# Optimization experiments

Measured on AMD Instinct MI355X. Metric: run time of the kernel, lower is better.

The kernel has to match this reference:

```python
import jax, jax.numpy as jnp
import numpy as np

CH = 256  # channels

def setup_inputs() -> dict:
    key = jax.random.key(0)
    ks = jax.random.split(key, 9)
    B, H, W = 8, 64, 64
    c8, c2 = CH // 8, CH // 2
    s = lambda fan_in: 1.0 / np.sqrt(fan_in)
    return {
        "x": jax.random.normal(ks[0], (B, H, W, CH), dtype=jnp.float32),
        "Wq": jax.random.normal(ks[1], (CH, c8), dtype=jnp.float32) * s(CH),
        "bq": jnp.zeros((c8,), dtype=jnp.float32),
        "Wk": jax.random.normal(ks[2], (CH, c8), dtype=jnp.float32) * s(CH),
        "bk": jnp.zeros((c8,), dtype=jnp.float32),
        "Wv": jax.random.normal(ks[3], (CH, c2), dtype=jnp.float32) * s(CH),
        "bv": jnp.zeros((c2,), dtype=jnp.float32),
        "Wo": jax.random.normal(ks[4], (c2, CH), dtype=jnp.float32) * s(c2),
        "bo": jnp.zeros((CH,), dtype=jnp.float32),
    }

def reference(x, Wq, bq, Wk, bk, Wv, bv, Wo, bo):
    B, H, W, C = x.shape
    # 1x1 convs are per-pixel matmuls over the channel dim
    q = x @ Wq + bq                      # [B,H,W,C/8]
    k = x @ Wk + bk                      # [B,H,W,C/8]
    v = x @ Wv + bv                      # [B,H,W,C/2]
    N = H * W
    qf = q.reshape(B, N, -1)
    kf = k.reshape(B, N, -1)
    vf = v.reshape(B, N, -1)
    # full self-attention over flattened spatial positions (no scaling, per source)
    scores = jnp.einsum('bnd,bmd->bnm', qf, kf)   # [B,N,N]
    attn = jax.nn.softmax(scores, axis=-1)
    out = jnp.einsum('bnm,bmd->bnd', attn, vf)    # [B,N,C/2]
    out = out.reshape(B, H, W, -1)
    return out @ Wo + bo + x
```

## Files before the change

### kernel.cpp

```cpp
#include <hip/hip_runtime.h>

typedef __attribute__((ext_vector_type(8))) short short8;
typedef __attribute__((ext_vector_type(4))) float f32x4;
typedef __attribute__((ext_vector_type(16))) float f32x16;

__device__ __forceinline__ unsigned short f2bf(float f) {
  unsigned int u = __float_as_uint(f);
  u += 0x7fffu + ((u >> 16) & 1u);
  return (unsigned short)(u >> 16);
}
__device__ __forceinline__ float bf2f(unsigned short h) {
  return __uint_as_float(((unsigned int)h) << 16);
}
__device__ __forceinline__ unsigned int cvtpk(float a, float b) {
  unsigned int r;
  asm("v_cvt_pk_bf16_f32 %0, %1, %2" : "=v"(r) : "v"(a), "v"(b));
  return r;
}
__device__ __forceinline__ float lo16f(unsigned int u) { return __uint_as_float(u << 16); }
__device__ __forceinline__ float hi16f(unsigned int u) { return __uint_as_float(u & 0xffff0000u); }
__device__ __forceinline__ short8 ld8(const unsigned short* p) {
  return *(const short8*)p;
}
__device__ __forceinline__ int swap23(int x) {
  return (x & 0x13) | ((x & 4) << 1) | ((x & 8) >> 1);
}
#define MFMA(a, b, c) __builtin_amdgcn_mfma_f32_16x16x32_bf16((a), (b), (c), 0, 0, 0)
#define MFMA32(a, b, c) __builtin_amdgcn_mfma_f32_32x32x16_bf16((a), (b), (c), 0, 0, 0)
#define LOG2E 1.4426950408889634f

typedef const __attribute__((address_space(1))) unsigned int* gas_u32p;
typedef __attribute__((address_space(3))) unsigned int* las_u32p;

__global__ void prep_weights(const float* __restrict__ Wq, const float* __restrict__ Wk,
                             const float* __restrict__ Wv, const float* __restrict__ Wo,
                             unsigned short* __restrict__ Wth, unsigned short* __restrict__ Wtl,
                             unsigned short* __restrict__ WoT) {
  int idx = blockIdx.x * 256 + threadIdx.x;
  if (idx < 192 * 256) {
    int o = idx >> 8, c = idx & 255;
    float w = (o < 32) ? Wq[c * 32 + o] : (o < 64) ? Wk[c * 32 + (o - 32)] : Wv[c * 128 + (o - 64)];
    unsigned short h = f2bf(w);
    Wth[idx] = h;
    Wtl[idx] = f2bf(w - bf2f(h));
  } else if (idx < 192 * 256 + 256 * 128) {
    int j = idx - 192 * 256;
    int c = j >> 7, d = j & 127;
    WoT[j] = f2bf(Wo[d * 256 + c]);
  }
}

__global__ __launch_bounds__(256) void proj_qkv(
    const float* __restrict__ x,
    const unsigned short* __restrict__ Wth, const unsigned short* __restrict__ Wtl,
    const float* __restrict__ bq, const float* __restrict__ bk, const float* __restrict__ bv,
    unsigned short* __restrict__ qh, unsigned short* __restrict__ qlo,
    unsigned short* __restrict__ KVF) {
  __shared__ unsigned short xsh[32][264];
  __shared__ unsigned short xsl[32][264];
  const int pix0 = blockIdx.x * 32;
  const int b = pix0 >> 12;
  const int nloc0 = pix0 & 4095;
  const int tid = threadIdx.x;

#pragma unroll
  for (int i = 0; i < 8; ++i) {
    int chunk = i * 256 + tid;
    int row = chunk >> 6;
    int c4 = (chunk & 63) * 4;
    float4 v = *(const float4*)(x + (size_t)(pix0 + row) * 256 + c4);
    unsigned int h01 = cvtpk(v.x, v.y), h23 = cvtpk(v.z, v.w);
    unsigned int l01 = cvtpk(v.x - lo16f(h01), v.y - hi16f(h01));
    unsigned int l23 = cvtpk(v.z - lo16f(h23), v.w - hi16f(h23));
    uint2 hp, lp;
    hp.x = h01; hp.y = h23;
    lp.x = l01; lp.y = l23;
    *(uint2*)&xsh[row][c4] = hp;
    *(uint2*)&xsl[row][c4] = lp;
  }
  __syncthreads();

  const int wave = tid >> 6, lane = tid & 63, l = lane & 15, qd = lane >> 4;
#pragma unroll
  for (int si = 0; si < 3; ++si) {
    const int sub = wave + si * 4;
    const int outc0 = sub * 16;
    if (si == 0) {
      const int outc = outc0 + l;
      const float bias = (outc < 32) ? bq[outc] : bk[outc - 32];
      f32x4 acc[2];
      acc[0] = (f32x4){bias, bias, bias, bias};
      acc[1] = (f32x4){bias, bias, bias, bias};
#pragma unroll
      for (int kc = 0; kc < 8; ++kc) {
        short8 whf = ld8(Wth + (size_t)(outc0 + l) * 256 + kc * 32 + qd * 8);
        short8 wlf = ld8(Wtl + (size_t)(outc0 + l) * 256 + kc * 32 + qd * 8);
#pragma unroll
        for (int m = 0; m < 2; ++m) {
          short8 xhf = ld8(&xsh[m * 16 + l][kc * 32 + qd * 8]);
          short8 xlf = ld8(&xsl[m * 16 + l][kc * 32 + qd * 8]);
          acc[m] = MFMA(xlf, whf, acc[m]);
          acc[m] = MFMA(xhf, wlf, acc[m]);
          acc[m] = MFMA(xhf, whf, acc[m]);
        }
      }
      if (outc < 32) {
#pragma unroll
        for (int m = 0; m < 2; ++m)
#pragma unroll
          for (int r = 0; r < 4; ++r) {
            const size_t pixel = (size_t)pix0 + m * 16 + 4 * qd + r;
            float val = acc[m][r] * LOG2E;
            unsigned int hp = cvtpk(val, val);
            float res = val - lo16f(hp);
            qh[pixel * 32 + outc] = (unsigned short)hp;
            qlo[pixel * 32 + outc] = (unsigned short)cvtpk(res, res);
          }
      } else {
        const int kd = outc - 32;
        const int step = kd >> 4, hh = (kd >> 3) & 1, e = kd & 7;
#pragma unroll
        for (int m = 0; m < 2; ++m)
#pragma unroll
          for (int r = 0; r < 4; ++r) {
            const int nl = nloc0 + m * 16 + 4 * qd + r;
            const int nt = nl >> 6, j = nl & 63, kt = j >> 5;
            const int lpos = swap23(j & 31);
            const size_t koff = (size_t)(b * 64 + nt) * 12288 +
                                (kt * 2 + step) * 512 + (hh * 32 + lpos) * 8 + e;
            float val = acc[m][r];
            unsigned int hp = cvtpk(val, val);
            float res = val - lo16f(hp);
            KVF[koff] = (unsigned short)hp;
            KVF[koff + 2048] = (unsigned short)cvtpk(res, res);
          }
      }
    } else {
      const int dv0 = outc0 - 64;
      const float b0 = bv[dv0 + 4 * qd + 0], b1 = bv[dv0 + 4 * qd + 1];
      const float b2 = bv[dv0 + 4 * qd + 2], b3 = bv[dv0 + 4 * qd + 3];
      f32x4 acc[2];
      acc[0] = (f32x4){b0, b1, b2, b3};
      acc[1] = (f32x4){b0, b1, b2, b3};
#pragma unroll
      for (int kc = 0; kc < 8; ++kc) {
        short8 whf = ld8(Wth + (size_t)(outc0 + l) * 256 + kc * 32 + qd * 8);
#pragma unroll
        for (int m = 0; m < 2; ++m) {
          short8 xhf = ld8(&xsh[m * 16 + l][kc * 32 + qd * 8]);
          acc[m] = MFMA(whf, xhf, acc[m]);
        }
      }
#pragma unroll
      for (int m = 0; m < 2; ++m)
#pragma unroll
        for (int r = 0; r < 4; ++r) {
          const int dv = dv0 + 4 * qd + r;
          const int dt = dv >> 5, lam = dv & 31;
          const int nl = nloc0 + m * 16 + l;
          const int nt = nl >> 6, j = nl & 63;
          const int ks = j >> 4, hh = (j >> 3) & 1, e = j & 7;
          const size_t voff = (size_t)(b * 64 + nt) * 12288 + 4096 +
                              (dt * 4 + ks) * 512 + (hh * 32 + lam) * 8 + e;
          KVF[voff] = (unsigned short)cvtpk(acc[m][r], acc[m][r]);
        }
    }
  }
}

__device__ __forceinline__ void stage_kv(const unsigned short* __restrict__ src,
                                         unsigned short* dst, int wave, int lane) {
#pragma unroll
  for (int i = 0; i < 6; ++i) {
    const int c = wave * 6 + i;
    __builtin_amdgcn_global_load_lds(
        (gas_u32p)(const void*)(src + c * 512 + lane * 8),
        (las_u32p)(void*)(dst + c * 512), 16, 0, 0);
  }
}

__global__ __launch_bounds__(256, 3) void flash_attn(
    const unsigned short* __restrict__ qh, const unsigned short* __restrict__ qlo,
    const unsigned short* __restrict__ KVF, unsigned short* __restrict__ opart,
    float* __restrict__ lstat) {
  __shared__ unsigned short kv[2][12288];
  const int b = blockIdx.x & 7;
  const int r7 = blockIdx.x >> 3;
  const int tile = r7 & 31;
  const int split = r7 >> 5;
  const int wave = threadIdx.x >> 6;
  const int lane = threadIdx.x & 63;
  const int lam = lane & 31;
  const int h = lane >> 5;
  const int m0 = tile * 128 + wave * 32;
  const int nt_begin = (split * 64 + 2) / 3;
  const int nt_end = ((split + 1) * 64 + 2) / 3;

  const unsigned short* qh_b = qh + (size_t)b * 4096 * 32;
  const unsigned short* ql_b = qlo + (size_t)b * 4096 * 32;
  const unsigned short* kv_b = KVF + (size_t)b * 64 * 12288;

  short8 qhf[2], qlf[2];
#pragma unroll
  for (int step = 0; step < 2; ++step) {
    size_t off = (size_t)(m0 + lam) * 32 + step * 16 + h * 8;
    qhf[step] = ld8(qh_b + off);
    qlf[step] = ld8(ql_b + off);
  }

  f32x16 acc[4];
#pragma unroll
  for (int dt = 0; dt < 4; ++dt)
#pragma unroll
    for (int e = 0; e < 16; ++e) acc[dt][e] = 0.f;
  float lr0 = 0.f, lr1 = 0.f;

  stage_kv(kv_b + (size_t)nt_begin * 12288, &kv[0][0], wave, lane);
  __syncthreads();

  int cur = 0;
#pragma unroll 1
  for (int it = nt_begin; it < nt_end; ++it) {
    if (it + 1 < nt_end)
      stage_kv(kv_b + (size_t)(it + 1) * 12288, &kv[cur ^ 1][0], wave, lane);

    const unsigned short* cb = &kv[cur][0];
#pragma unroll
    for (int kt = 0; kt < 2; ++kt) {
      f32x16 z;
#pragma unroll
      for (int e = 0; e < 16; ++e) z[e] = 0.f;
#pragma unroll
      for (int step = 0; step < 2; ++step) {
        short8 khf = *(const short8*)(cb + (kt * 2 + step) * 512 + lane * 8);
        short8 klf = *(const short8*)(cb + 2048 + (kt * 2 + step) * 512 + lane * 8);
        z = MFMA32(klf, qhf[step], z);
        z = MFMA32(khf, qlf[step], z);
        z = MFMA32(khf, qhf[step], z);
      }
      unsigned int pp[8];
#pragma unroll
      for (int g = 0; g < 8; ++g) {
        float p0 = __builtin_amdgcn_exp2f(z[2 * g]);
        float p1 = __builtin_amdgcn_exp2f(z[2 * g + 1]);
        lr0 += p0;
        lr1 += p1;
        pp[g] = cvtpk(p0, p1);
      }
#pragma unroll
      for (int kss = 0; kss < 2; ++kss) {
        union { unsigned int u[4]; short8 v; } pf;
        pf.u[0] = pp[4 * kss + 0];
        pf.u[1] = pp[4 * kss + 1];
        pf.u[2] = pp[4 * kss + 2];
        pf.u[3] = pp[4 * kss + 3];
        const int ks = kt * 2 + kss;
#pragma unroll
        for (int dt = 0; dt < 4; ++dt) {
          short8 vfrag = *(const short8*)(cb + 4096 + (dt * 4 + ks) * 512 + lane * 8);
          acc[dt] = MFMA32(vfrag, pf.v, acc[dt]);
        }
      }
    }
    __syncthreads();
    cur ^= 1;
  }

  const float lrun = lr0 + lr1;
  const float ltot = lrun + __shfl_xor(lrun, 32);
  const int grow = b * 4096 + m0 + lam;
  if (h == 0) lstat[split * 32768 + grow] = ltot;
  const size_t obase = ((size_t)split * 32768 + grow) * 128;
#pragma unroll
  for (int dt = 0; dt < 4; ++dt)
#pragma unroll
    for (int g = 0; g < 8; ++g) {
      int r = 2 * g;
      int dv = dt * 32 + (r & 3) + 8 * (r >> 2) + 4 * h;
      *(unsigned int*)(opart + obase + dv) = cvtpk(acc[dt][r], acc[dt][r + 1]);
    }
}

__global__ __launch_bounds__(256) void combine_splits(
    const unsigned short* __restrict__ opart, const float* __restrict__ lstat,
    unsigned short* __restrict__ ao) {
  const int tid = threadIdx.x;
  const int row = blockIdx.x * 16 + (tid >> 4);
  const int col = (tid & 15) * 8;
  float den = lstat[row] + lstat[32768 + row] + lstat[65536 + row];
  float inv = 1.f / den;
  float o[8] = {0.f, 0.f, 0.f, 0.f, 0.f, 0.f, 0.f, 0.f};
#pragma unroll
  for (int s = 0; s < 3; ++s) {
    uint4 v = *(const uint4*)(opart + ((size_t)s * 32768 + row) * 128 + col);
    unsigned int uu[4] = {v.x, v.y, v.z, v.w};
#pragma unroll
    for (int j = 0; j < 4; ++j) {
      o[2 * j]     += bf2f((unsigned short)(uu[j] & 0xffff));
      o[2 * j + 1] += bf2f((unsigned short)(uu[j] >> 16));
    }
  }
  uint4 outv;
  outv.x = cvtpk(o[0] * inv, o[1] * inv);
  outv.y = cvtpk(o[2] * inv, o[3] * inv);
  outv.z = cvtpk(o[4] * inv, o[5] * inv);
  outv.w = cvtpk(o[6] * inv, o[7] * inv);
  *(uint4*)(ao + (size_t)row * 128 + col) = outv;
}

__global__ __launch_bounds__(256) void out_proj(
    const unsigned short* __restrict__ ao, const unsigned short* __restrict__ WoT,
    const float* __restrict__ bo, const float* __restrict__ x, float* __restrict__ out) {
  const int pix0 = blockIdx.x * 64;
  const int wave = threadIdx.x >> 6, lane = threadIdx.x & 63, l = lane & 15, qd = lane >> 4;
  const int base = pix0 + wave * 16;
  short8 af[4];
#pragma unroll
  for (int kc = 0; kc < 4; ++kc)
    af[kc] = ld8(ao + (size_t)(base + l) * 128 + kc * 32 + qd * 8);
#pragma unroll
  for (int sub = 0; sub < 16; ++sub) {
    const int c = sub * 16 + l;
    const float bias = bo[c];
    f32x4 acc = (f32x4){bias, bias, bias, bias};
#pragma unroll
    for (int kc = 0; kc < 4; ++kc) {
      short8 wf = ld8(WoT + (size_t)c * 128 + kc * 32 + qd * 8);
      acc = MFMA(af[kc], wf, acc);
    }
#pragma unroll
    for (int r = 0; r < 4; ++r) {
      const size_t pixel = (size_t)base + 4 * qd + r;
      out[pixel * 256 + c] = acc[r] + x[pixel * 256 + c];
    }
  }
}

extern "C" void kernel_launch(void* const* d_in, const int* in_sizes, int n_in,
                              void* d_out, int out_size, void* d_ws, size_t ws_size,
                              hipStream_t stream) {
  const float* x  = (const float*)d_in[0];
  const float* Wq = (const float*)d_in[1];
  const float* bq = (const float*)d_in[2];
  const float* Wk = (const float*)d_in[3];
  const float* bk = (const float*)d_in[4];
  const float* Wv = (const float*)d_in[5];
  const float* bv = (const float*)d_in[6];
  const float* Wo = (const float*)d_in[7];
  const float* bo = (const float*)d_in[8];

  char* ws = (char*)d_ws;
  unsigned short* qh  = (unsigned short*)(ws + 0);
  unsigned short* qlo = (unsigned short*)(ws + 2097152);
  unsigned short* KVF = (unsigned short*)(ws + 4194304);
  unsigned short* ao  = (unsigned short*)(ws + 16777216);
  unsigned short* Wth = (unsigned short*)(ws + 25165824);
  unsigned short* Wtl = (unsigned short*)(ws + 25264128);
  unsigned short* WoT = (unsigned short*)(ws + 25362432);
  float*          lst = (float*)(ws + 25493504);
  unsigned short* opart = (unsigned short*)d_out;

  prep_weights<<<320, 256, 0, stream>>>(Wq, Wk, Wv, Wo, Wth, Wtl, WoT);
  proj_qkv<<<1024, 256, 0, stream>>>(x, Wth, Wtl, bq, bk, bv, qh, qlo, KVF);
  flash_attn<<<768, 256, 0, stream>>>(qh, qlo, KVF, opart, lst);
  combine_splits<<<2048, 256, 0, stream>>>(opart, lst, ao);
  out_proj<<<512, 256, 0, stream>>>(ao, WoT, bo, x, (float*)d_out);
}
```

Measured before the change: 196.1 us.

## Process two query tiles per wave in flash attention and vectorize out_proj stores

Each wave now handles 64 query rows (two 32-row tiles), so every K/V fragment read from LDS feeds twice as many MFMAs. The grid moves from 3 splits of 128-row tiles to 4 splits of 256-row tiles, with combine_splits updated to sum four partials. MFMA sections are wrapped in s_setprio. out_proj swaps the MFMA operands so each lane holds 4 consecutive channels, allowing float4 bias, residual and output accesses. In exchange, register pressure rises (occupancy hint drops from 3 to 2 blocks), fewer blocks are launched, and the workspace traffic for partials grows.

```diff
diff --git a/kernel.cpp b/kernel.cpp
--- a/kernel.cpp
+++ b/kernel.cpp
@@ -1,6 +1,7 @@
 #include <hip/hip_runtime.h>
 
 typedef __attribute__((ext_vector_type(8))) short short8;
+typedef __attribute__((ext_vector_type(2))) float f32x2;
 typedef __attribute__((ext_vector_type(4))) float f32x4;
 typedef __attribute__((ext_vector_type(16))) float f32x16;
 
@@ -179,106 +180,143 @@
   }
 }
 
-__global__ __launch_bounds__(256, 3) void flash_attn(
+__global__ __launch_bounds__(256, 2) void flash_attn(
     const unsigned short* __restrict__ qh, const unsigned short* __restrict__ qlo,
     const unsigned short* __restrict__ KVF, unsigned short* __restrict__ opart,
     float* __restrict__ lstat) {
   __shared__ unsigned short kv[2][12288];
   const int b = blockIdx.x & 7;
   const int r7 = blockIdx.x >> 3;
-  const int tile = r7 & 31;
-  const int split = r7 >> 5;
+  const int tile = r7 & 15;
+  const int split = r7 >> 4;
   const int wave = threadIdx.x >> 6;
   const int lane = threadIdx.x & 63;
   const int lam = lane & 31;
   const int h = lane >> 5;
-  const int m0 = tile * 128 + wave * 32;
-  const int nt_begin = (split * 64 + 2) / 3;
-  const int nt_end = ((split + 1) * 64 + 2) / 3;
+  const int m0 = tile * 256 + wave * 64;
+  const int nt0 = split * 16;
 
   const unsigned short* qh_b = qh + (size_t)b * 4096 * 32;
   const unsigned short* ql_b = qlo + (size_t)b * 4096 * 32;
   const unsigned short* kv_b = KVF + (size_t)b * 64 * 12288;
 
-  short8 qhf[2], qlf[2];
-#pragma unroll
-  for (int step = 0; step < 2; ++step) {
-    size_t off = (size_t)(m0 + lam) * 32 + step * 16 + h * 8;
-    qhf[step] = ld8(qh_b + off);
-    qlf[step] = ld8(ql_b + off);
-  }
-
-  f32x16 acc[4];
+  short8 qhf[2][2], qlf[2][2];
+#pragma unroll
+  for (int t = 0; t < 2; ++t)
+#pragma unroll
+    for (int step = 0; step < 2; ++step) {
+      size_t off = (size_t)(m0 + t * 32 + lam) * 32 + step * 16 + h * 8;
+      qhf[t][step] = ld8(qh_b + off);
+      qlf[t][step] = ld8(ql_b + off);
+    }
+
+  f32x16 acc0[4], acc1[4];
 #pragma unroll
   for (int dt = 0; dt < 4; ++dt)
 #pragma unroll
-    for (int e = 0; e < 16; ++e) acc[dt][e] = 0.f;
-  float lr0 = 0.f, lr1 = 0.f;
-
-  stage_kv(kv_b + (size_t)nt_begin * 12288, &kv[0][0], wave, lane);
+    for (int e = 0; e < 16; ++e) { acc0[dt][e] = 0.f; acc1[dt][e] = 0.f; }
+  f32x2 lr0 = (f32x2){0.f, 0.f}, lr1 = (f32x2){0.f, 0.f};
+
+  stage_kv(kv_b + (size_t)nt0 * 12288, &kv[0][0], wave, lane);
   __syncthreads();
 
   int cur = 0;
 #pragma unroll 1
-  for (int it = nt_begin; it < nt_end; ++it) {
-    if (it + 1 < nt_end)
-      stage_kv(kv_b + (size_t)(it + 1) * 12288, &kv[cur ^ 1][0], wave, lane);
+  for (int it = 0; it < 16; ++it) {
+    if (it < 15)
+      stage_kv(kv_b + (size_t)(nt0 + it + 1) * 12288, &kv[cur ^ 1][0], wave, lane);
 
     const unsigned short* cb = &kv[cur][0];
 #pragma unroll
     for (int kt = 0; kt < 2; ++kt) {
-      f32x16 z;
-#pragma unroll
-      for (int e = 0; e < 16; ++e) z[e] = 0.f;
+      short8 khf[2], klf[2];
 #pragma unroll
       for (int step = 0; step < 2; ++step) {
-        short8 khf = *(const short8*)(cb + (kt * 2 + step) * 512 + lane * 8);
-        short8 klf = *(const short8*)(cb + 2048 + (kt * 2 + step) * 512 + lane * 8);
-        z = MFMA32(klf, qhf[step], z);
-        z = MFMA32(khf, qlf[step], z);
-        z = MFMA32(khf, qhf[step], z);
-      }
-      unsigned int pp[8];
+        khf[step] = *(const short8*)(cb + (kt * 2 + step) * 512 + lane * 8);
+        klf[step] = *(const short8*)(cb + 2048 + (kt * 2 + step) * 512 + lane * 8);
+      }
+      f32x16 z0, z1;
+#pragma unroll
+      for (int e = 0; e < 16; ++e) { z0[e] = 0.f; z1[e] = 0.f; }
+      __builtin_amdgcn_s_setprio(1);
+#pragma unroll
+      for (int step = 0; step < 2; ++step) {
+        z0 = MFMA32(klf[step], qhf[0][step], z0);
+        z0 = MFMA32(khf[step], qlf[0][step], z0);
+        z0 = MFMA32(khf[step], qhf[0][step], z0);
+      }
+#pragma unroll
+      for (int step = 0; step < 2; ++step) {
+        z1 = MFMA32(klf[step], qhf[1][step], z1);
+        z1 = MFMA32(khf[step], qlf[1][step], z1);
+        z1 = MFMA32(khf[step], qhf[1][step], z1);
+      }
+      __builtin_amdgcn_s_setprio(0);
+      unsigned int pp0[8], pp1[8];
 #pragma unroll
       for (int g = 0; g < 8; ++g) {
-        float p0 = __builtin_amdgcn_exp2f(z[2 * g]);
-        float p1 = __builtin_amdgcn_exp2f(z[2 * g + 1]);
-        lr0 += p0;
-        lr1 += p1;
-        pp[g] = cvtpk(p0, p1);
-      }
+        float a0 = __builtin_amdgcn_exp2f(z0[2 * g]);
+        float a1 = __builtin_amdgcn_exp2f(z0[2 * g + 1]);
+        lr0 += (f32x2){a0, a1};
+        pp0[g] = cvtpk(a0, a1);
+        float c0 = __builtin_amdgcn_exp2f(z1[2 * g]);
+        float c1 = __builtin_amdgcn_exp2f(z1[2 * g + 1]);
+        lr1 += (f32x2){c0, c1};
+        pp1[g] = cvtpk(c0, c1);
+      }
+      __builtin_amdgcn_s_setprio(1);
 #pragma unroll
       for (int kss = 0; kss < 2; ++kss) {
-        union { unsigned int u[4]; short8 v; } pf;
-        pf.u[0] = pp[4 * kss + 0];
-        pf.u[1] = pp[4 * kss + 1];
-        pf.u[2] = pp[4 * kss + 2];
-        pf.u[3] = pp[4 * kss + 3];
+        union { unsigned int u[4]; short8 v; } pf0, pf1;
+#pragma unroll
+        for (int j = 0; j < 4; ++j) {
+          pf0.u[j] = pp0[4 * kss + j];
+          pf1.u[j] = pp1[4 * kss + j];
+        }
         const int ks = kt * 2 + kss;
 #pragma unroll
         for (int dt = 0; dt < 4; ++dt) {
           short8 vfrag = *(const short8*)(cb + 4096 + (dt * 4 + ks) * 512 + lane * 8);
-          acc[dt] = MFMA32(vfrag, pf.v, acc[dt]);
+          acc0[dt] = MFMA32(vfrag, pf0.v, acc0[dt]);
+          acc1[dt] = MFMA32(vfrag, pf1.v, acc1[dt]);
         }
       }
+      __builtin_amdgcn_s_setprio(0);
     }
     __syncthreads();
     cur ^= 1;
   }
 
-  const float lrun = lr0 + lr1;
-  const float ltot = lrun + __shfl_xor(lrun, 32);
-  const int grow = b * 4096 + m0 + lam;
-  if (h == 0) lstat[split * 32768 + grow] = ltot;
-  const size_t obase = ((size_t)split * 32768 + grow) * 128;
-#pragma unroll
-  for (int dt = 0; dt < 4; ++dt)
-#pragma unroll
-    for (int g = 0; g < 8; ++g) {
-      int r = 2 * g;
-      int dv = dt * 32 + (r & 3) + 8 * (r >> 2) + 4 * h;
-      *(unsigned int*)(opart + obase + dv) = cvtpk(acc[dt][r], acc[dt][r + 1]);
-    }
+  {
+    const float lrun = lr0.x + lr0.y;
+    const float ltot = lrun + __shfl_xor(lrun, 32);
+    const int grow = b * 4096 + m0 + lam;
+    if (h == 0) lstat[split * 32768 + grow] = ltot;
+    const size_t obase = ((size_t)split * 32768 + grow) * 128;
+#pragma unroll
+    for (int dt = 0; dt < 4; ++dt)
+#pragma unroll
+      for (int g = 0; g < 8; ++g) {
+        int r = 2 * g;
+        int dv = dt * 32 + (r & 3) + 8 * (r >> 2) + 4 * h;
+        *(unsigned int*)(opart + obase + dv) = cvtpk(acc0[dt][r], acc0[dt][r + 1]);
+      }
+  }
+  {
+    const float lrun = lr1.x + lr1.y;
+    const float ltot = lrun + __shfl_xor(lrun, 32);
+    const int grow = b * 4096 + m0 + 32 + lam;
+    if (h == 0) lstat[split * 32768 + grow] = ltot;
+    const size_t obase = ((size_t)split * 32768 + grow) * 128;
+#pragma unroll
+    for (int dt = 0; dt < 4; ++dt)
+#pragma unroll
+      for (int g = 0; g < 8; ++g) {
+        int r = 2 * g;
+        int dv = dt * 32 + (r & 3) + 8 * (r >> 2) + 4 * h;
+        *(unsigned int*)(opart + obase + dv) = cvtpk(acc1[dt][r], acc1[dt][r + 1]);
+      }
+  }
 }
 
 __global__ __launch_bounds__(256) void combine_splits(
@@ -287,11 +325,11 @@
   const int tid = threadIdx.x;
   const int row = blockIdx.x * 16 + (tid >> 4);
   const int col = (tid & 15) * 8;
-  float den = lstat[row] + lstat[32768 + row] + lstat[65536 + row];
+  float den = lstat[row] + lstat[32768 + row] + lstat[65536 + row] + lstat[98304 + row];
   float inv = 1.f / den;
   float o[8] = {0.f, 0.f, 0.f, 0.f, 0.f, 0.f, 0.f, 0.f};
 #pragma unroll
-  for (int s = 0; s < 3; ++s) {
+  for (int s = 0; s < 4; ++s) {
     uint4 v = *(const uint4*)(opart + ((size_t)s * 32768 + row) * 128 + col);
     unsigned int uu[4] = {v.x, v.y, v.z, v.w};
 #pragma unroll
@@ -320,19 +358,21 @@
     af[kc] = ld8(ao + (size_t)(base + l) * 128 + kc * 32 + qd * 8);
 #pragma unroll
   for (int sub = 0; sub < 16; ++sub) {
-    const int c = sub * 16 + l;
-    const float bias = bo[c];
-    f32x4 acc = (f32x4){bias, bias, bias, bias};
+    const int c0 = sub * 16 + 4 * qd;
+    float4 bb = *(const float4*)(bo + c0);
+    f32x4 acc = (f32x4){bb.x, bb.y, bb.z, bb.w};
 #pragma unroll
     for (int kc = 0; kc < 4; ++kc) {
-      short8 wf = ld8(WoT + (size_t)c * 128 + kc * 32 + qd * 8);
-      acc = MFMA(af[kc], wf, acc);
+      short8 wf = ld8(WoT + (size_t)(sub * 16 + l) * 128 + kc * 32 + qd * 8);
+      acc = MFMA(wf, af[kc], acc);
     }
-#pragma unroll
-    for (int r = 0; r < 4; ++r) {
-      const size_t pixel = (size_t)base + 4 * qd + r;
-      out[pixel * 256 + c] = acc[r] + x[pixel * 256 + c];
-    }
+    float4 xv = *(const float4*)(x + (size_t)(base + l) * 256 + c0);
+    float4 res;
+    res.x = acc[0] + xv.x;
+    res.y = acc[1] + xv.y;
+    res.z = acc[2] + xv.z;
+    res.w = acc[3] + xv.w;
+    *(float4*)(out + (size_t)(base + l) * 256 + c0) = res;
   }
 }
 
@@ -362,7 +402,7 @@
 
   prep_weights<<<320, 256, 0, stream>>>(Wq, Wk, Wv, Wo, Wth, Wtl, WoT);
   proj_qkv<<<1024, 256, 0, stream>>>(x, Wth, Wtl, bq, bk, bv, qh, qlo, KVF);
-  flash_attn<<<768, 256, 0, stream>>>(qh, qlo, KVF, opart, lst);
+  flash_attn<<<512, 256, 0, stream>>>(qh, qlo, KVF, opart, lst);
   combine_splits<<<2048, 256, 0, stream>>>(opart, lst, ao);
   out_proj<<<512, 256, 0, stream>>>(ao, WoT, bo, x, (float*)d_out);
 }
```

Result: slower. 200.4 us (+2.2%).
